# Kernel optimization log

Measured on AMD Instinct MI355X. Metric: run time of the kernel, lower is better.

The kernel has to match this reference:

```python
import jax, jax.numpy as jnp
import numpy as np

N_NODES = 100000
N_EDGES = 3200000
DROP_P = 0.5


def gcn_conv(x, W, b, src, dst, deg_inv_sqrt, n):
    # PyG GCNConv with self-loops already folded into (src, dst):
    # out[j] = sum_{(i->j)} dinv[i]*dinv[j] * (x W)[i] + b
    h = x @ W
    norm = deg_inv_sqrt[src] * deg_inv_sqrt[dst]          # [E+N]
    msg = h[src] * norm[:, None]                          # [E+N, d_out]
    out = jax.ops.segment_sum(msg, dst, num_segments=n)
    return out + b


def dropout(x, key, p=DROP_P):
    keep = jax.random.bernoulli(key, 1.0 - p, x.shape)
    return jnp.where(keep, x / (1.0 - p), 0.0)


def setup_inputs() -> dict:
    key = jax.random.key(0)
    ks = jax.random.split(key, 8)
    x = jax.random.normal(ks[0], (N_NODES, 64), dtype=jnp.float32)
    edge_index = jax.random.randint(ks[1], (2, N_EDGES), 0, N_NODES, dtype=jnp.int64)
    def glorot(k, fin, fout):
        lim = float(np.sqrt(6.0 / (fin + fout)))
        return jax.random.uniform(k, (fin, fout), jnp.float32, -lim, lim)
    return {
        "x": x,
        "edge_index": edge_index,
        "W1": glorot(ks[2], 64, 32), "b1": jnp.zeros((32,), jnp.float32),
        "W2": glorot(ks[3], 32, 64), "b2": jnp.zeros((64,), jnp.float32),
        "W3": glorot(ks[4], 64, 32), "b3": jnp.zeros((32,), jnp.float32),
    }


def reference(x, edge_index, W1, b1, W2, b2, W3, b3):
    n = x.shape[0]
    loops = jnp.arange(n, dtype=edge_index.dtype)
    src = jnp.concatenate([edge_index[0], loops])          # [E+N]
    dst = jnp.concatenate([edge_index[1], loops])
    deg = jax.ops.segment_sum(jnp.ones_like(dst, dtype=x.dtype), dst, num_segments=n)
    deg_inv_sqrt = jnp.where(deg > 0, jax.lax.rsqrt(deg), 0.0)

    dkey = jax.random.key(42)
    k1, k2 = jax.random.split(dkey)

    h = gcn_conv(x, W1, b1, src, dst, deg_inv_sqrt, n)
    h = jax.nn.celu(h)
    h = dropout(h, k1)
    h = gcn_conv(h, W2, b2, src, dst, deg_inv_sqrt, n)
    h = jax.nn.celu(h)
    h = dropout(h, k2)
    h = gcn_conv(h, W3, b3, src, dst, deg_inv_sqrt, n)
    return jax.nn.celu(h)
```

## Files before the change

### kernel.cpp

```cpp
#include <hip/hip_runtime.h>
#include <stdint.h>
#include <stddef.h>

typedef _Float16 half_t;
typedef _Float16 half4 __attribute__((ext_vector_type(4)));

__host__ __device__ __forceinline__ uint32_t rotl32(uint32_t v, uint32_t r) {
  return (v << r) | (v >> (32u - r));
}

__host__ __device__ __forceinline__ void tf2x32(uint32_t k0, uint32_t k1,
                                                uint32_t x0, uint32_t x1,
                                                uint32_t& o0, uint32_t& o1) {
  uint32_t ks2 = k0 ^ k1 ^ 0x1BD11BDAu;
  x0 += k0; x1 += k1;
  x0 += x1; x1 = rotl32(x1, 13); x1 ^= x0;
  x0 += x1; x1 = rotl32(x1, 15); x1 ^= x0;
  x0 += x1; x1 = rotl32(x1, 26); x1 ^= x0;
  x0 += x1; x1 = rotl32(x1, 6);  x1 ^= x0;
  x0 += k1; x1 += ks2 + 1u;
  x0 += x1; x1 = rotl32(x1, 17); x1 ^= x0;
  x0 += x1; x1 = rotl32(x1, 29); x1 ^= x0;
  x0 += x1; x1 = rotl32(x1, 16); x1 ^= x0;
  x0 += x1; x1 = rotl32(x1, 24); x1 ^= x0;
  x0 += ks2; x1 += k0 + 2u;
  x0 += x1; x1 = rotl32(x1, 13); x1 ^= x0;
  x0 += x1; x1 = rotl32(x1, 15); x1 ^= x0;
  x0 += x1; x1 = rotl32(x1, 26); x1 ^= x0;
  x0 += x1; x1 = rotl32(x1, 6);  x1 ^= x0;
  x0 += k0; x1 += k1 + 3u;
  x0 += x1; x1 = rotl32(x1, 17); x1 ^= x0;
  x0 += x1; x1 = rotl32(x1, 29); x1 ^= x0;
  x0 += x1; x1 = rotl32(x1, 16); x1 ^= x0;
  x0 += x1; x1 = rotl32(x1, 24); x1 ^= x0;
  x0 += k1; x1 += ks2 + 4u;
  x0 += x1; x1 = rotl32(x1, 13); x1 ^= x0;
  x0 += x1; x1 = rotl32(x1, 15); x1 ^= x0;
  x0 += x1; x1 = rotl32(x1, 26); x1 ^= x0;
  x0 += x1; x1 = rotl32(x1, 6);  x1 ^= x0;
  x0 += ks2; x1 += k0 + 5u;
  o0 = x0; o1 = x1;
}

__device__ __forceinline__ bool tf_keep(uint32_t k0, uint32_t k1, uint32_t idx) {
  uint32_t o0, o1;
  tf2x32(k0, k1, 0u, idx, o0, o1);
  return ((o0 ^ o1) >> 31) == 0u;
}

#define CHUNK 4096
#define STASH 5120

__global__ __launch_bounds__(1024) void zero1024(uint32_t* __restrict__ p) {
  p[threadIdx.x] = 0u;
}

__global__ __launch_bounds__(256) void k4_binhist(const int* __restrict__ src,
                                                  const int* __restrict__ dst,
                                                  uint32_t* __restrict__ tbl,
                                                  uint32_t* __restrict__ gbcnt,
                                                  uint32_t* __restrict__ staging,
                                                  int E, int NB) {
  __shared__ uint32_t lcur[1024];
  __shared__ uint32_t ls[256];
  __shared__ uint32_t stage[CHUNK];
  int tid = threadIdx.x;
  for (int i = tid; i < NB; i += 256) lcur[i] = 0u;
  __syncthreads();
  int base = blockIdx.x * CHUNK;
  int end = min(base + CHUNK, E);
  uint32_t dv[16], sv[16];
  int m = 0;
  for (int i = base + tid; i < end; i += 256) {
    dv[m] = (uint32_t)dst[i];
    sv[m] = (uint32_t)src[i];
    ++m;
  }
  for (int q = 0; q < m; ++q) atomicAdd(&lcur[dv[q] >> 7], 1u);
  __syncthreads();
  uint32_t carry = 0u;
  for (int seg = 0; seg < 1024; seg += 256) {
    int i = seg + tid;
    uint32_t v = (i < NB) ? lcur[i] : 0u;
    ls[tid] = v;
    __syncthreads();
    for (int off = 1; off < 256; off <<= 1) {
      uint32_t t = (tid >= off) ? ls[tid - off] : 0u;
      __syncthreads();
      if (tid >= off) ls[tid] += t;
      __syncthreads();
    }
    uint32_t excl = carry + ls[tid] - v;
    if (i < NB) {
      tbl[(size_t)blockIdx.x * NB + i] = (excl << 16) | v;
      if (v) atomicAdd(&gbcnt[i], v);
      lcur[i] = excl;
    }
    carry += ls[255];
    __syncthreads();
  }
  for (int q = 0; q < m; ++q) {
    uint32_t d = dv[q];
    uint32_t p = atomicAdd(&lcur[d >> 7], 1u);
    stage[p] = ((d & 127u) << 17) | sv[q];
  }
  __syncthreads();
  int cnt_total = end - base;
  uint32_t* outp = staging + (size_t)blockIdx.x * CHUNK;
  for (int i = tid; i < cnt_total; i += 256) outp[i] = stage[i];
}

__global__ __launch_bounds__(1024) void k3_bscan(const uint32_t* __restrict__ gbcnt,
                                                 uint32_t* __restrict__ bbase, int NB) {
  __shared__ uint32_t s[1024];
  int i = threadIdx.x;
  uint32_t v = (i < NB) ? gbcnt[i] : 0u;
  s[i] = v;
  __syncthreads();
  for (int off = 1; off < 1024; off <<= 1) {
    uint32_t t = (i >= off) ? s[i - off] : 0u;
    __syncthreads();
    if (i >= off) s[i] += t;
    __syncthreads();
  }
  if (i < NB) bbase[i] = s[i] - v;
}

__global__ __launch_bounds__(256) void k5_fin(
    const uint32_t* __restrict__ staging, const uint32_t* __restrict__ tbl,
    const uint32_t* __restrict__ bbase, uint32_t* __restrict__ rowp,
    float* __restrict__ dinv, uint32_t* __restrict__ esrc,
    int n, int E, int NBLK, int NB) {
  __shared__ uint32_t lpak[1024];
  __shared__ uint32_t P[1025];
  __shared__ uint32_t ls[256];
  __shared__ uint32_t stash[STASH];
  __shared__ uint32_t lc[128];
  __shared__ uint32_t sc[128];
  __shared__ uint32_t lcur[128];
  int tid = threadIdx.x;
  int b = blockIdx.x;
  if (tid < 128) lc[tid] = 0u;
  uint32_t carry = 0u;
  for (int seg = 0; seg < 1024; seg += 256) {
    int i = seg + tid;
    uint32_t packed = (i < NBLK) ? tbl[(size_t)i * NB + b] : 0u;
    lpak[i] = packed;
    uint32_t v = packed & 0xFFFFu;
    ls[tid] = v;
    __syncthreads();
    for (int off = 1; off < 256; off <<= 1) {
      uint32_t t = (tid >= off) ? ls[tid - off] : 0u;
      __syncthreads();
      if (tid >= off) ls[tid] += t;
      __syncthreads();
    }
    P[i] = carry + ls[tid] - v;
    carry += ls[255];
    __syncthreads();
  }
  if (tid == 0) P[NBLK] = carry;
  __syncthreads();
  uint32_t total = P[NBLK];
  for (int i = tid; i < NBLK; i += 256) {
    uint32_t packed = lpak[i];
    uint32_t cnt = packed & 0xFFFFu;
    uint32_t loff = packed >> 16;
    uint32_t p = P[i];
    const uint32_t* run = staging + (size_t)i * CHUNK + loff;
    for (uint32_t t2 = 0; t2 < cnt; ++t2) {
      uint32_t e = run[t2];
      uint32_t q = p + t2;
      if (q < STASH) stash[q] = e;
      atomicAdd(&lc[e >> 17], 1u);
    }
  }
  __syncthreads();
  uint32_t myc = (tid < 128) ? lc[tid] : 0u;
  if (tid < 128) sc[tid] = myc;
  __syncthreads();
  for (int off = 1; off < 128; off <<= 1) {
    uint32_t t = (tid < 128 && tid >= off) ? sc[tid - off] : 0u;
    __syncthreads();
    if (tid < 128 && tid >= off) sc[tid] += t;
    __syncthreads();
  }
  uint32_t s = bbase[b];
  if (tid < 128) {
    uint32_t gstart = s + sc[tid] - myc;
    int node = (b << 7) + tid;
    if (node < n) {
      rowp[node] = gstart;
      dinv[node] = 1.0f / sqrtf((float)(myc + 1u));
    }
    lcur[tid] = gstart;
  }
  if (b == 0 && tid == 0) rowp[n] = (uint32_t)E;
  __syncthreads();
  uint32_t lim = total < (uint32_t)STASH ? total : (uint32_t)STASH;
  for (uint32_t q = tid; q < lim; q += 256) {
    uint32_t e = stash[q];
    uint32_t pos = atomicAdd(&lcur[e >> 17], 1u);
    esrc[pos] = e & 0x1FFFFu;
  }
  if (total > (uint32_t)STASH) {
    for (int i = tid; i < NBLK; i += 256) {
      uint32_t packed = lpak[i];
      uint32_t cnt = packed & 0xFFFFu;
      uint32_t loff = packed >> 16;
      uint32_t p = P[i];
      const uint32_t* run = staging + (size_t)i * CHUNK + loff;
      for (uint32_t t2 = 0; t2 < cnt; ++t2) {
        uint32_t q = p + t2;
        if (q >= (uint32_t)STASH) {
          uint32_t e = run[t2];
          uint32_t pos = atomicAdd(&lcur[e >> 17], 1u);
          esrc[pos] = e & 0x1FFFFu;
        }
      }
    }
  }
}

__global__ __launch_bounds__(256) void gemm_n64_k32(
    const float* __restrict__ X, const float* __restrict__ W,
    const float* __restrict__ dinv, half_t* __restrict__ out16, int n) {
  __shared__ float Ws[64 * 32];
  __shared__ float Xs[32 * 68];
  int tid = threadIdx.x;
  {
    const float4* Wv = (const float4*)W;
    float4* Wsv = (float4*)Ws;
    Wsv[tid] = Wv[tid];
    Wsv[tid + 256] = Wv[tid + 256];
  }
  int row0 = blockIdx.x * 32;
  {
    const float4* Xv = (const float4*)(X + (size_t)row0 * 64);
    int lim = (n - row0) * 16;
    float4 z = make_float4(0.f, 0.f, 0.f, 0.f);
    int i0 = tid, i1 = tid + 256;
    float4 v0 = (i0 < lim) ? Xv[i0] : z;
    float4 v1 = (i1 < lim) ? Xv[i1] : z;
    *(float4*)(Xs + (i0 >> 4) * 68 + ((i0 & 15) << 2)) = v0;
    *(float4*)(Xs + (i1 >> 4) * 68 + ((i1 & 15) << 2)) = v1;
  }
  __syncthreads();
  int r = tid >> 3;
  int c4 = (tid & 7) << 2;
  int row = row0 + r;
  if (row >= n) return;
  float4 acc = make_float4(0.f, 0.f, 0.f, 0.f);
#pragma unroll
  for (int k = 0; k < 64; k += 4) {
    float4 xv = *(const float4*)(Xs + r * 68 + k);
    float4 w0 = *(const float4*)(Ws + (k + 0) * 32 + c4);
    float4 w1 = *(const float4*)(Ws + (k + 1) * 32 + c4);
    float4 w2 = *(const float4*)(Ws + (k + 2) * 32 + c4);
    float4 w3 = *(const float4*)(Ws + (k + 3) * 32 + c4);
    acc.x = fmaf(xv.x, w0.x, acc.x); acc.y = fmaf(xv.x, w0.y, acc.y);
    acc.z = fmaf(xv.x, w0.z, acc.z); acc.w = fmaf(xv.x, w0.w, acc.w);
    acc.x = fmaf(xv.y, w1.x, acc.x); acc.y = fmaf(xv.y, w1.y, acc.y);
    acc.z = fmaf(xv.y, w1.z, acc.z); acc.w = fmaf(xv.y, w1.w, acc.w);
    acc.x = fmaf(xv.z, w2.x, acc.x); acc.y = fmaf(xv.z, w2.y, acc.y);
    acc.z = fmaf(xv.z, w2.z, acc.z); acc.w = fmaf(xv.z, w2.w, acc.w);
    acc.x = fmaf(xv.w, w3.x, acc.x); acc.y = fmaf(xv.w, w3.y, acc.y);
    acc.z = fmaf(xv.w, w3.z, acc.z); acc.w = fmaf(xv.w, w3.w, acc.w);
  }
  float dj = dinv[row];
  half4 h;
  h.x = (half_t)(acc.x * dj); h.y = (half_t)(acc.y * dj);
  h.z = (half_t)(acc.z * dj); h.w = (half_t)(acc.w * dj);
  size_t slab = (size_t)(c4 >> 4) * ((size_t)n * 16);
  *(half4*)(out16 + slab + (size_t)row * 16 + (c4 & 15)) = h;
}

__global__ __launch_bounds__(256) void gemm_k32_n64_act(
    const float* __restrict__ X, const float* __restrict__ W,
    const float* __restrict__ bias, float* __restrict__ out,
    uint32_t k0, uint32_t k1, int n) {
  __shared__ float Ws[32 * 64];
  __shared__ float Xs[16 * 36];
  int tid = threadIdx.x;
  {
    const float4* Wv = (const float4*)W;
    float4* Wsv = (float4*)Ws;
    Wsv[tid] = Wv[tid];
    Wsv[tid + 256] = Wv[tid + 256];
  }
  int row0 = blockIdx.x * 16;
  if (tid < 128) {
    const float4* Xv = (const float4*)(X + (size_t)row0 * 32);
    int lim = (n - row0) * 8;
    float4 z = make_float4(0.f, 0.f, 0.f, 0.f);
    float4 v = (tid < lim) ? Xv[tid] : z;
    *(float4*)(Xs + (tid >> 3) * 36 + ((tid & 7) << 2)) = v;
  }
  __syncthreads();
  int r = tid >> 4;
  int c4 = (tid & 15) << 2;
  int row = row0 + r;
  if (row >= n) return;
  float4 acc = make_float4(0.f, 0.f, 0.f, 0.f);
#pragma unroll
  for (int k = 0; k < 32; k += 4) {
    float4 xv = *(const float4*)(Xs + r * 36 + k);
    float4 w0 = *(const float4*)(Ws + (k + 0) * 64 + c4);
    float4 w1 = *(const float4*)(Ws + (k + 1) * 64 + c4);
    float4 w2 = *(const float4*)(Ws + (k + 2) * 64 + c4);
    float4 w3 = *(const float4*)(Ws + (k + 3) * 64 + c4);
    acc.x = fmaf(xv.x, w0.x, acc.x); acc.y = fmaf(xv.x, w0.y, acc.y);
    acc.z = fmaf(xv.x, w0.z, acc.z); acc.w = fmaf(xv.x, w0.w, acc.w);
    acc.x = fmaf(xv.y, w1.x, acc.x); acc.y = fmaf(xv.y, w1.y, acc.y);
    acc.z = fmaf(xv.y, w1.z, acc.z); acc.w = fmaf(xv.y, w1.w, acc.w);
    acc.x = fmaf(xv.z, w2.x, acc.x); acc.y = fmaf(xv.z, w2.y, acc.y);
    acc.z = fmaf(xv.z, w2.z, acc.z); acc.w = fmaf(xv.z, w2.w, acc.w);
    acc.x = fmaf(xv.w, w3.x, acc.x); acc.y = fmaf(xv.w, w3.y, acc.y);
    acc.z = fmaf(xv.w, w3.z, acc.z); acc.w = fmaf(xv.w, w3.w, acc.w);
  }
  float4 bv = *(const float4*)(bias + c4);
  float vv[4] = {acc.x + bv.x, acc.y + bv.y, acc.z + bv.z, acc.w + bv.w};
  uint32_t base = (uint32_t)row * 64u + (uint32_t)c4;
#pragma unroll
  for (int q = 0; q < 4; ++q) {
    float v = vv[q];
    v = v > 0.f ? v : expm1f(v);
    vv[q] = tf_keep(k0, k1, base + q) ? v * 2.f : 0.f;
  }
  *(float4*)(out + (size_t)row * 64 + c4) = make_float4(vv[0], vv[1], vv[2], vv[3]);
}

__global__ __launch_bounds__(256) void gather_fin(
    const half_t* __restrict__ hs, const uint32_t* __restrict__ rowp,
    const uint32_t* __restrict__ esrc, const float* __restrict__ dinv,
    const float* __restrict__ bias, float* __restrict__ outf,
    half_t* __restrict__ outh, int n, int mode, uint32_t k0, uint32_t k1,
    float fone) {
  uint32_t bid = blockIdx.x;
  int cg = (int)((bid >> 2) & 1u);
  int dstblk = (int)((bid >> 3) * 4u + (bid & 3u));
  int tid = threadIdx.x;
  int j = dstblk * 8 + (tid >> 5);
  if (j >= n) return;
  int l = tid & 31;
  int eslot = l >> 2;
  int chunk = l & 3;
  const half_t* slab = hs + (size_t)cg * ((size_t)n * 16);
  float4 acc = make_float4(0.f, 0.f, 0.f, 0.f);
  uint32_t e0 = rowp[j], e1 = rowp[j + 1];
  uint32_t deg = e1 - e0;
  uint32_t base = 0;
  for (; base + 32 <= deg; base += 32) {
    uint32_t idx = esrc[e0 + base + (uint32_t)l];
#pragma unroll
    for (int k = 0; k < 32; k += 8) {
      uint32_t s = (uint32_t)__shfl((int)idx, k + eslot, 32);
      const half4 v = *(const half4*)(slab + (size_t)s * 16 + (chunk << 2));
      acc.x = fmaf((float)v.x, fone, acc.x);
      acc.y = fmaf((float)v.y, fone, acc.y);
      acc.z = fmaf((float)v.z, fone, acc.z);
      acc.w = fmaf((float)v.w, fone, acc.w);
    }
  }
  if (base < deg) {
    uint32_t rem = deg - base;
    uint32_t li = (uint32_t)l < rem ? (uint32_t)l : rem - 1u;
    uint32_t idx = esrc[e0 + base + li];
    for (uint32_t k = 0; k < rem; k += 8) {
      uint32_t kk = k + (uint32_t)eslot;
      uint32_t ks = kk < rem ? kk : rem - 1u;
      uint32_t s = (uint32_t)__shfl((int)idx, (int)ks, 32);
      if (kk < rem) {
        const half4 v = *(const half4*)(slab + (size_t)s * 16 + (chunk << 2));
        acc.x = fmaf((float)v.x, fone, acc.x);
        acc.y = fmaf((float)v.y, fone, acc.y);
        acc.z = fmaf((float)v.z, fone, acc.z);
        acc.w = fmaf((float)v.w, fone, acc.w);
      }
    }
  }
  acc.x += __shfl_xor(acc.x, 4);  acc.y += __shfl_xor(acc.y, 4);
  acc.z += __shfl_xor(acc.z, 4);  acc.w += __shfl_xor(acc.w, 4);
  acc.x += __shfl_xor(acc.x, 8);  acc.y += __shfl_xor(acc.y, 8);
  acc.z += __shfl_xor(acc.z, 8);  acc.w += __shfl_xor(acc.w, 8);
  acc.x += __shfl_xor(acc.x, 16); acc.y += __shfl_xor(acc.y, 16);
  acc.z += __shfl_xor(acc.z, 16); acc.w += __shfl_xor(acc.w, 16);
  float va = __shfl(acc.x, l >> 2, 32);
  float vb = __shfl(acc.y, l >> 2, 32);
  float vc = __shfl(acc.z, l >> 2, 32);
  float vd = __shfl(acc.w, l >> 2, 32);
  if (l >= 16) return;
  float lo = (l & 1) ? vb : va;
  float hi = (l & 1) ? vd : vc;
  float sum = (l & 2) ? hi : lo;
  sum += (float)slab[(size_t)j * 16 + l];
  int c = (cg << 4) | l;
  float dj = dinv[j];
  float v = dj * sum;
  if (mode == 1) {
    v += bias[c];
    v = v > 0.f ? v : expm1f(v);
    outf[(size_t)j * 32 + c] = v;
  } else if (mode == 3) {
    v += bias[c];
    v = v > 0.f ? v : expm1f(v);
    v = tf_keep(k0, k1, (uint32_t)(j * 32 + c)) ? v * 2.f : 0.f;
    v *= dj;
    outh[(size_t)cg * ((size_t)n * 16) + (size_t)j * 16 + l] = (half_t)v;
  } else {
    outf[(size_t)j * 32 + c] = v;
  }
}

extern "C" void kernel_launch(void* const* d_in, const int* in_sizes, int n_in,
                              void* d_out, int out_size, void* d_ws, size_t ws_size,
                              hipStream_t stream) {
  const float* x  = (const float*)d_in[0];
  const int*   ei = (const int*)d_in[1];
  const float* W1 = (const float*)d_in[2];
  const float* b1 = (const float*)d_in[3];
  const float* W2 = (const float*)d_in[4];
  const float* b2 = (const float*)d_in[5];
  const float* W3 = (const float*)d_in[6];
  const float* b3 = (const float*)d_in[7];
  float* out = (float*)d_out;

  const int n = in_sizes[0] / 64;
  const int E = in_sizes[1] / 2;
  const int* src = ei;
  const int* dst = ei + E;

  char* ws = (char*)d_ws;
  size_t off = 0;
  auto alloc = [&](size_t bytes) {
    void* p = ws + off;
    off = (off + bytes + 255) & ~(size_t)255;
    return p;
  };
  float*    A32   = (float*)alloc((size_t)n * 32 * 4);
  float*    C     = (float*)alloc((size_t)n * 64 * 4);
  half_t*   A16   = (half_t*)alloc((size_t)n * 32 * 2);
  half_t*   B16   = (half_t*)alloc((size_t)n * 32 * 2);
  float*    dinv  = (float*)alloc((size_t)n * 4);
  uint32_t* rowp  = (uint32_t*)alloc((size_t)(n + 1) * 4);
  uint32_t* esrc  = (uint32_t*)alloc((size_t)E * 4);
  uint32_t* gbcnt = (uint32_t*)alloc(1024 * 4);
  uint32_t* bbase = (uint32_t*)alloc(1024 * 4);
  uint32_t* staging = (uint32_t*)C;
  uint32_t* tbl     = (uint32_t*)A32;
  (void)ws_size; (void)n_in; (void)out_size;

  uint32_t k1a, k1b, k2a, k2b;
  tf2x32(0u, 42u, 0u, 0u, k1a, k1b);
  tf2x32(0u, 42u, 0u, 1u, k2a, k2b);

  const int NB   = (n + 127) >> 7;
  const int NBLK = (E + CHUNK - 1) / CHUNK;
  const int NDB  = (n + 7) / 8;
  const int gV2  = 8 * ((NDB + 3) / 4 + 1);
  const int gG1  = (n + 31) / 32;
  const int gG2  = (n + 15) / 16;
  dim3 blk(256);

  zero1024<<<1, dim3(1024), 0, stream>>>(gbcnt);
  k4_binhist<<<NBLK, blk, 0, stream>>>(src, dst, tbl, gbcnt, staging, E, NB);
  k3_bscan<<<1, dim3(1024), 0, stream>>>(gbcnt, bbase, NB);
  k5_fin<<<NB, blk, 0, stream>>>(staging, tbl, bbase, rowp, dinv, esrc, n, E, NBLK, NB);

  gemm_n64_k32<<<gG1, blk, 0, stream>>>(x, W1, dinv, A16, n);
  gather_fin<<<gV2, blk, 0, stream>>>(A16, rowp, esrc, dinv, b1, nullptr, B16, n, 3, k1a, k1b, 1.0f);

  gather_fin<<<gV2, blk, 0, stream>>>(B16, rowp, esrc, dinv, nullptr, A32, nullptr, n, 0, 0u, 0u, 1.0f);
  gemm_k32_n64_act<<<gG2, blk, 0, stream>>>(A32, W2, b2, C, k2a, k2b, n);

  gemm_n64_k32<<<gG1, blk, 0, stream>>>(C, W3, dinv, A16, n);
  gather_fin<<<gV2, blk, 0, stream>>>(A16, rowp, esrc, dinv, b3, out, nullptr, n, 1, 0u, 0u, 1.0f);
}
```

Baseline: 385.7 us.

## Stage edge indices in LDS and gather half8 rows per lane

The gather kernel now cooperatively loads the CSR source indices for its block's 8 destination nodes into shared memory, falling back to global reads when they exceed capacity. Each lane then fetches a 16-byte half8 chunk instead of half4, with 16 edges in flight per warp-group, replacing shuffle-based index broadcast. The cross-lane reduction goes through an LDS buffer, and the grid drops one excess block group. It adds 24KB of LDS per block, which may lower occupancy, plus a block-wide barrier.

```diff
diff --git a/kernel.cpp b/kernel.cpp
--- a/kernel.cpp
+++ b/kernel.cpp
@@ -4,6 +4,7 @@
 
 typedef _Float16 half_t;
 typedef _Float16 half4 __attribute__((ext_vector_type(4)));
+typedef _Float16 half8 __attribute__((ext_vector_type(8)));
 
 __host__ __device__ __forceinline__ uint32_t rotl32(uint32_t v, uint32_t r) {
   return (v << r) | (v >> (32u - r));
@@ -330,69 +331,73 @@
   *(float4*)(out + (size_t)row * 64 + c4) = make_float4(vv[0], vv[1], vv[2], vv[3]);
 }
 
+#define ECAP 6144
+
 __global__ __launch_bounds__(256) void gather_fin(
     const half_t* __restrict__ hs, const uint32_t* __restrict__ rowp,
     const uint32_t* __restrict__ esrc, const float* __restrict__ dinv,
     const float* __restrict__ bias, float* __restrict__ outf,
     half_t* __restrict__ outh, int n, int mode, uint32_t k0, uint32_t k1,
     float fone) {
+  __shared__ uint32_t ldsidx[ECAP];
+  __shared__ __align__(16) float ldsred[8 * 16];
   uint32_t bid = blockIdx.x;
   int cg = (int)((bid >> 2) & 1u);
   int dstblk = (int)((bid >> 3) * 4u + (bid & 3u));
   int tid = threadIdx.x;
-  int j = dstblk * 8 + (tid >> 5);
-  if (j >= n) return;
+  int j0 = dstblk * 8;
+  if (j0 >= n) return;
+  int jend = min(j0 + 8, n);
+  uint32_t e0blk = rowp[j0];
+  uint32_t esz = rowp[jend] - e0blk;
+  bool fits = esz <= (uint32_t)ECAP;
+  if (fits) {
+    for (uint32_t i = (uint32_t)tid; i < esz; i += 256u)
+      ldsidx[i] = esrc[e0blk + i];
+  }
+  __syncthreads();
+  int g = tid >> 5;
+  int j = j0 + g;
   int l = tid & 31;
-  int eslot = l >> 2;
-  int chunk = l & 3;
+  int eslot = l >> 1;
+  int chunk = l & 1;
   const half_t* slab = hs + (size_t)cg * ((size_t)n * 16);
-  float4 acc = make_float4(0.f, 0.f, 0.f, 0.f);
-  uint32_t e0 = rowp[j], e1 = rowp[j + 1];
-  uint32_t deg = e1 - e0;
-  uint32_t base = 0;
-  for (; base + 32 <= deg; base += 32) {
-    uint32_t idx = esrc[e0 + base + (uint32_t)l];
-#pragma unroll
-    for (int k = 0; k < 32; k += 8) {
-      uint32_t s = (uint32_t)__shfl((int)idx, k + eslot, 32);
-      const half4 v = *(const half4*)(slab + (size_t)s * 16 + (chunk << 2));
-      acc.x = fmaf((float)v.x, fone, acc.x);
-      acc.y = fmaf((float)v.y, fone, acc.y);
-      acc.z = fmaf((float)v.z, fone, acc.z);
-      acc.w = fmaf((float)v.w, fone, acc.w);
-    }
-  }
-  if (base < deg) {
-    uint32_t rem = deg - base;
-    uint32_t li = (uint32_t)l < rem ? (uint32_t)l : rem - 1u;
-    uint32_t idx = esrc[e0 + base + li];
-    for (uint32_t k = 0; k < rem; k += 8) {
-      uint32_t kk = k + (uint32_t)eslot;
-      uint32_t ks = kk < rem ? kk : rem - 1u;
-      uint32_t s = (uint32_t)__shfl((int)idx, (int)ks, 32);
-      if (kk < rem) {
-        const half4 v = *(const half4*)(slab + (size_t)s * 16 + (chunk << 2));
-        acc.x = fmaf((float)v.x, fone, acc.x);
-        acc.y = fmaf((float)v.y, fone, acc.y);
-        acc.z = fmaf((float)v.z, fone, acc.z);
-        acc.w = fmaf((float)v.w, fone, acc.w);
+  float acc[8] = {0.f, 0.f, 0.f, 0.f, 0.f, 0.f, 0.f, 0.f};
+  if (j < n) {
+    uint32_t e0 = rowp[j], e1 = rowp[j + 1];
+    uint32_t deg = e1 - e0;
+    uint32_t eloc = e0 - e0blk;
+    const half_t* hp = slab + (size_t)(chunk << 3);
+    if (fits) {
+      for (uint32_t e = (uint32_t)eslot; e < deg; e += 16u) {
+        uint32_t idx = ldsidx[eloc + e];
+        const half8 v = *(const half8*)(hp + ((size_t)idx << 4));
+#pragma unroll
+        for (int q = 0; q < 8; ++q) acc[q] = fmaf((float)v[q], fone, acc[q]);
       }
-    }
-  }
-  acc.x += __shfl_xor(acc.x, 4);  acc.y += __shfl_xor(acc.y, 4);
-  acc.z += __shfl_xor(acc.z, 4);  acc.w += __shfl_xor(acc.w, 4);
-  acc.x += __shfl_xor(acc.x, 8);  acc.y += __shfl_xor(acc.y, 8);
-  acc.z += __shfl_xor(acc.z, 8);  acc.w += __shfl_xor(acc.w, 8);
-  acc.x += __shfl_xor(acc.x, 16); acc.y += __shfl_xor(acc.y, 16);
-  acc.z += __shfl_xor(acc.z, 16); acc.w += __shfl_xor(acc.w, 16);
-  float va = __shfl(acc.x, l >> 2, 32);
-  float vb = __shfl(acc.y, l >> 2, 32);
-  float vc = __shfl(acc.z, l >> 2, 32);
-  float vd = __shfl(acc.w, l >> 2, 32);
-  if (l >= 16) return;
-  float lo = (l & 1) ? vb : va;
-  float hi = (l & 1) ? vd : vc;
-  float sum = (l & 2) ? hi : lo;
+    } else {
+      for (uint32_t e = (uint32_t)eslot; e < deg; e += 16u) {
+        uint32_t idx = esrc[e0 + e];
+        const half8 v = *(const half8*)(hp + ((size_t)idx << 4));
+#pragma unroll
+        for (int q = 0; q < 8; ++q) acc[q] = fmaf((float)v[q], fone, acc[q]);
+      }
+    }
+  }
+#pragma unroll
+  for (int m = 2; m <= 16; m <<= 1) {
+#pragma unroll
+    for (int q = 0; q < 8; ++q) acc[q] += __shfl_xor(acc[q], m);
+  }
+  if (l < 2) {
+    *(float4*)(&ldsred[(g << 4) + (chunk << 3) + 0]) =
+        make_float4(acc[0], acc[1], acc[2], acc[3]);
+    *(float4*)(&ldsred[(g << 4) + (chunk << 3) + 4]) =
+        make_float4(acc[4], acc[5], acc[6], acc[7]);
+  }
+  __builtin_amdgcn_wave_barrier();
+  if (l >= 16 || j >= n) return;
+  float sum = ldsred[(g << 4) + l];
   sum += (float)slab[(size_t)j * 16 + l];
   int c = (cg << 4) | l;
   float dj = dinv[j];
@@ -457,7 +462,7 @@
   const int NB   = (n + 127) >> 7;
   const int NBLK = (E + CHUNK - 1) / CHUNK;
   const int NDB  = (n + 7) / 8;
-  const int gV2  = 8 * ((NDB + 3) / 4 + 1);
+  const int gV2  = 8 * ((NDB + 3) / 4);
   const int gG1  = (n + 31) / 32;
   const int gG2  = (n + 15) / 16;
   dim3 blk(256);
```

After: 411.0 us. 1.07x slower.
